# Kernel tuning notes

Measured on AMD Instinct MI355X. Metric: run time of the kernel, lower is better.

Reference implementation:

```python
import jax, jax.numpy as jnp
import numpy as np

B, L, D = 4, 1024, 1024
H, DK, DV = 16, 64, 64
HID = 4 * D
EPS = 1e-5


def layer_norm(x, w, b):
    m = x.mean(-1, keepdims=True)
    v = ((x - m) ** 2).mean(-1, keepdims=True)
    return (x - m) * jax.lax.rsqrt(v + EPS) * w + b


def sln(hl, w, ln_w, ln_b, gamma, beta):
    # Self-modulated LayerNorm: gamma * w * LN(hl) + beta * w
    return gamma * w * layer_norm(hl, ln_w, ln_b) + beta * w


def setup_inputs() -> dict:
    key = jax.random.key(0)
    ks = jax.random.split(key, 20)
    s = 0.02
    inp = {
        "q": jax.random.normal(ks[0], (B, L, D), jnp.float32),
        "k": jax.random.normal(ks[1], (B, L, D), jnp.float32),
        "v": jax.random.normal(ks[2], (B, L, D), jnp.float32),
        "z": jax.random.normal(ks[3], (B, L, D), jnp.float32),
        # projections stored [in, out] (torch Linear applies x @ W.T + b)
        "wq_w": jax.random.normal(ks[4], (D, H * DK), jnp.float32) * s,
        "wq_b": jnp.zeros((H * DK,), jnp.float32),
        "wk_w": jax.random.normal(ks[5], (D, H * DK), jnp.float32) * s,
        "wk_b": jnp.zeros((H * DK,), jnp.float32),
        "wv_w": jax.random.normal(ks[6], (D, H * DV), jnp.float32) * s,
        "wv_b": jnp.zeros((H * DV,), jnp.float32),
        "fc_w": jax.random.normal(ks[7], (H * DV, D), jnp.float32) * s,
        "fc_b": jnp.zeros((D,), jnp.float32),
        "mlp1_w": jax.random.normal(ks[8], (D, HID), jnp.float32) * s,
        "mlp1_b": jnp.zeros((HID,), jnp.float32),
        "mlp2_w": jax.random.normal(ks[9], (HID, D), jnp.float32) * s,
        "mlp2_b": jnp.zeros((D,), jnp.float32),
        "ln1_w": jnp.ones((D,), jnp.float32),
        "ln1_b": jnp.zeros((D,), jnp.float32),
        "g1": jax.random.normal(ks[10], (1, 1, 1), jnp.float32),
        "b1": jax.random.normal(ks[11], (1, 1, 1), jnp.float32),
        "ln2_w": jnp.ones((D,), jnp.float32),
        "ln2_b": jnp.zeros((D,), jnp.float32),
        "g2": jax.random.normal(ks[12], (1, 1, 1), jnp.float32),
        "b2": jax.random.normal(ks[13], (1, 1, 1), jnp.float32),
    }
    return inp


def reference(q, k, v, z,
              wq_w, wq_b, wk_w, wk_b, wv_w, wv_b, fc_w, fc_b,
              mlp1_w, mlp1_b, mlp2_w, mlp2_b,
              ln1_w, ln1_b, g1, b1, ln2_w, ln2_b, g2, b2):
    scale = 1.0 / np.sqrt(DK).astype(np.float32)
    q = sln(q, z, ln1_w, ln1_b, g1, b1)
    residual = q
    qh = (q @ wq_w + wq_b).reshape(B, L, H, DK)
    kh = (k @ wk_w + wk_b).reshape(B, L, H, DK)
    vh = (v @ wv_w + wv_b).reshape(B, L, H, DV)
    # scores per (head, batch) matching torch layout (n_head*sz_b, Lq, Lk)
    attn = jnp.einsum("bqhd,bkhd->hbqk", qh, kh) * scale
    attn = jax.nn.softmax(attn, axis=-1)
    out = jnp.einsum("hbqk,bkhd->bqhd", attn, vh).reshape(B, L, H * DV)
    out = out @ fc_w + fc_b
    out = out + residual
    h = sln(out, z, ln2_w, ln2_b, g2, b2)
    h = jax.nn.gelu(h @ mlp1_w + mlp1_b, approximate=False)
    out = (h @ mlp2_w + mlp2_b) + out
    return out, attn.reshape(H * B, L, L)
```

## Files before the change

### kernel.cpp

```cpp
#include <hip/hip_runtime.h>
#include <math.h>

namespace {

constexpr int kL  = 1024;
constexpr int kD  = 1024;
constexpr int kB  = 4;
constexpr int kH  = 16;
constexpr int kDK = 64;
constexpr int kHID = 4096;

typedef unsigned short ushort_t;
typedef short  s16x8 __attribute__((ext_vector_type(8)));
typedef float  f32x4 __attribute__((ext_vector_type(4)));
typedef unsigned short u16x4 __attribute__((ext_vector_type(4)));

__device__ __forceinline__ ushort_t f2bf(float f) {
    unsigned u = __float_as_uint(f);
    unsigned r = u + 0x7fffu + ((u >> 16) & 1u);
    return (ushort_t)(r >> 16);
}

__device__ __forceinline__ void gld16(const void* g, void* l) {
    __builtin_amdgcn_global_load_lds((__attribute__((address_space(1))) void*)(g),
                                     (__attribute__((address_space(3))) void*)(l),
                                     16, 0, 0);
}

__device__ __forceinline__ float wred_sum(float v) {
    #pragma unroll
    for (int o = 32; o > 0; o >>= 1) v += __shfl_xor(v, o, 64);
    return v;
}

__global__ __launch_bounds__(256) void prep(
    const float* __restrict__ wq_w, const float* __restrict__ wk_w,
    const float* __restrict__ wv_w, const float* __restrict__ fc_w,
    ushort_t* __restrict__ wT4,
    const float* __restrict__ mlp1_w, ushort_t* __restrict__ m1T,
    const float* __restrict__ mlp2_w, ushort_t* __restrict__ m2T,
    const float* __restrict__ kx, const float* __restrict__ vx, ushort_t* __restrict__ kv,
    const float* __restrict__ q, const float* __restrict__ z,
    const float* __restrict__ ln1w, const float* __restrict__ ln1b,
    const float* __restrict__ g1, const float* __restrict__ b1,
    float* __restrict__ qp, ushort_t* __restrict__ qb)
{
    __shared__ float t[32][33];
    __shared__ float r1[4], r2[4];
    const int b = blockIdx.x;
    const int tid = threadIdx.x;
    if (b < 12288) {
        const float* src; ushort_t* dst; int R, C, bx, by;
        if (b < 4096) {
            int zz = b >> 10, idx = b & 1023;
            src = zz == 0 ? wq_w : zz == 1 ? wk_w : zz == 2 ? wv_w : fc_w;
            dst = wT4 + (size_t)zz * 1048576;
            R = 1024; C = 1024; bx = idx & 31; by = idx >> 5;
        } else if (b < 8192) {
            int idx = b - 4096;
            src = mlp1_w; dst = m1T; R = 1024; C = 4096;
            bx = idx & 127; by = idx >> 7;
        } else {
            int idx = b - 8192;
            src = mlp2_w; dst = m2T; R = 4096; C = 1024;
            bx = idx & 31; by = idx >> 5;
        }
        int c0 = bx * 32, rr0 = by * 32;
        int tx = tid & 31, ty = tid >> 5;
        #pragma unroll
        for (int i = 0; i < 4; i++) {
            int r = ty + i * 8;
            t[r][tx] = src[(size_t)(rr0 + r) * C + c0 + tx];
        }
        __syncthreads();
        #pragma unroll
        for (int i = 0; i < 4; i++) {
            int c = ty + i * 8;
            dst[(size_t)(c0 + c) * R + rr0 + tx] = f2bf(t[tx][c]);
        }
        return;
    }
    if (b < 20480) {
        int bb = b - 12288;
        bool isv = bb >= 4096;
        const float* src = isv ? vx : kx;
        ushort_t* dst = kv + (isv ? (size_t)4194304 : 0);
        int i = (bb & 4095) * 256 + tid;
        f32x4 v = ((const f32x4*)src)[i];
        u16x4 o; o[0] = f2bf(v[0]); o[1] = f2bf(v[1]); o[2] = f2bf(v[2]); o[3] = f2bf(v[3]);
        ((u16x4*)dst)[i] = o;
        return;
    }
    {
        const int row = b - 20480;
        const size_t base = (size_t)row * kD;
        float4 xv = ((const float4*)(q + base))[tid];
        float s  = xv.x + xv.y + xv.z + xv.w;
        float sq = xv.x * xv.x + xv.y * xv.y + xv.z * xv.z + xv.w * xv.w;
        float ws = wred_sum(s), wq = wred_sum(sq);
        int lane = tid & 63, wid = tid >> 6;
        if (lane == 0) { r1[wid] = ws; r2[wid] = wq; }
        __syncthreads();
        float st = r1[0] + r1[1] + r1[2] + r1[3];
        float qt = r2[0] + r2[1] + r2[2] + r2[3];
        float mean = st * (1.0f / kD);
        float var  = qt * (1.0f / kD) - mean * mean;
        float rs = rsqrtf(var + 1e-5f);
        float gv = g1[0], bv = b1[0];
        float4 zv = ((const float4*)(z + base))[tid];
        float4 wv = ((const float4*)ln1w)[tid];
        float4 lb = ((const float4*)ln1b)[tid];
        float4 o;
        o.x = zv.x * (gv * ((xv.x - mean) * rs * wv.x + lb.x) + bv);
        o.y = zv.y * (gv * ((xv.y - mean) * rs * wv.y + lb.y) + bv);
        o.z = zv.z * (gv * ((xv.z - mean) * rs * wv.z + lb.z) + bv);
        o.w = zv.w * (gv * ((xv.w - mean) * rs * wv.w + lb.w) + bv);
        ((float4*)(qp + base))[tid] = o;
        u16x4 ob; ob[0] = f2bf(o.x); ob[1] = f2bf(o.y); ob[2] = f2bf(o.z); ob[3] = f2bf(o.w);
        ((u16x4*)(qb + base))[tid] = ob;
    }
}

__global__ __launch_bounds__(256) void sln_kernel(
    const float* __restrict__ x, const float* __restrict__ x2, float* __restrict__ xw,
    const float* __restrict__ z,
    const float* __restrict__ lnw, const float* __restrict__ lnb,
    const float* __restrict__ g, const float* __restrict__ bt,
    float* __restrict__ outf, ushort_t* __restrict__ outb)
{
    const int row = blockIdx.x;
    const int tid = threadIdx.x;
    const size_t base = (size_t)row * kD;
    float4 xv = ((const float4*)(x + base))[tid];
    if (x2) {
        float4 a = ((const float4*)(x2 + base))[tid];
        xv.x += a.x; xv.y += a.y; xv.z += a.z; xv.w += a.w;
    }
    if (xw) ((float4*)(xw + base))[tid] = xv;
    float s  = xv.x + xv.y + xv.z + xv.w;
    float sq = xv.x * xv.x + xv.y * xv.y + xv.z * xv.z + xv.w * xv.w;
    __shared__ float r1[4], r2[4];
    float ws = wred_sum(s), wq = wred_sum(sq);
    int lane = tid & 63, wid = tid >> 6;
    if (lane == 0) { r1[wid] = ws; r2[wid] = wq; }
    __syncthreads();
    float st = r1[0] + r1[1] + r1[2] + r1[3];
    float qt = r2[0] + r2[1] + r2[2] + r2[3];
    float mean = st * (1.0f / kD);
    float var  = qt * (1.0f / kD) - mean * mean;
    float rs = rsqrtf(var + 1e-5f);
    float gv = g[0], bv = bt[0];
    float4 zv = ((const float4*)(z + base))[tid];
    float4 wv = ((const float4*)lnw)[tid];
    float4 lb = ((const float4*)lnb)[tid];
    float4 o;
    o.x = zv.x * (gv * ((xv.x - mean) * rs * wv.x + lb.x) + bv);
    o.y = zv.y * (gv * ((xv.y - mean) * rs * wv.y + lb.y) + bv);
    o.z = zv.z * (gv * ((xv.z - mean) * rs * wv.z + lb.z) + bv);
    o.w = zv.w * (gv * ((xv.w - mean) * rs * wv.w + lb.w) + bv);
    if (outf) ((float4*)(outf + base))[tid] = o;
    u16x4 ob; ob[0] = f2bf(o.x); ob[1] = f2bf(o.y); ob[2] = f2bf(o.z); ob[3] = f2bf(o.w);
    ((u16x4*)(outb + base))[tid] = ob;
}

__global__ __launch_bounds__(256) void combine4(
    float* __restrict__ dst, const float* __restrict__ p1,
    const float* __restrict__ p2, const float* __restrict__ p3)
{
    int i = blockIdx.x * 256 + threadIdx.x;
    f32x4 d = ((const f32x4*)dst)[i];
    f32x4 a = ((const f32x4*)p1)[i];
    f32x4 b = ((const f32x4*)p2)[i];
    f32x4 c = ((const f32x4*)p3)[i];
    d[0] += a[0] + b[0] + c[0]; d[1] += a[1] + b[1] + c[1];
    d[2] += a[2] + b[2] + c[2]; d[3] += a[3] + b[3] + c[3];
    ((f32x4*)dst)[i] = d;
}

__global__ __launch_bounds__(256) void vtrans(
    const ushort_t* __restrict__ vh, ushort_t* __restrict__ vhT)
{
    __shared__ ushort_t t[32][33];
    int p = blockIdx.z, b = p & 3, h = p >> 2;
    int j0 = blockIdx.x * 32, d0 = blockIdx.y * 32;
    int tx = threadIdx.x & 31, ty = threadIdx.x >> 5;
    const ushort_t* src = vh + (size_t)b * (kL * kD) + h * kDK;
    #pragma unroll
    for (int i = 0; i < 4; i++) {
        int j = ty + i * 8;
        t[j][tx] = src[(size_t)(j0 + j) * kD + d0 + tx];
    }
    __syncthreads();
    ushort_t* dst = vhT + (size_t)p * (kDK * kL);
    #pragma unroll
    for (int i = 0; i < 4; i++) {
        int d = ty + i * 8;
        dst[(size_t)(d0 + d) * kL + j0 + tx] = t[tx][d];
    }
}

__global__ __launch_bounds__(256) void mgemm(
    const ushort_t* __restrict__ A, int lda,
    const ushort_t* __restrict__ Bt, int ldb,
    void* __restrict__ Cv, int ldc, int K,
    const float* __restrict__ bias, const float* __restrict__ res,
    float scale, int flags, int mode,
    const float* __restrict__ bias1, const float* __restrict__ bias2,
    void* __restrict__ Cv2)
{
    __shared__ __align__(16) ushort_t As[128 * 32];
    __shared__ __align__(16) ushort_t Bs[128 * 32];
    if (mode == 3) {
        int z = blockIdx.z;
        A  += (size_t)z * K;
        Bt += (size_t)z * K;
        if (z == 1) { Cv = Cv2; bias = nullptr; res = nullptr; flags = 0; }
    }
    float*    Cf = (float*)Cv;
    ushort_t* Cb = (ushort_t*)Cv;
    const int nx = gridDim.x, nwg = nx * gridDim.y;
    int f = blockIdx.y * nx + blockIdx.x;
    int rr = (f & 7) * (nwg >> 3) + (f >> 3);
    const int bx = rr % nx, by = rr / nx;
    const int tid = threadIdx.x;
    const int lane = tid & 63, w = tid >> 6;
    const int m0 = by * 128, n0 = bx * 128;
    const int r0 = tid >> 2;
    const int c0 = (tid & 3) ^ (r0 & 3);
    const ushort_t* Ag0 = A  + (size_t)(m0 + r0) * lda + c0 * 8;
    const ushort_t* Ag1 = Ag0 + (size_t)64 * lda;
    const ushort_t* Bg0 = Bt + (size_t)(n0 + r0) * ldb + c0 * 8;
    const ushort_t* Bg1 = Bg0 + (size_t)64 * ldb;
    char* AsW = (char*)As + w * 1024;
    char* BsW = (char*)Bs + w * 1024;
    const int wm = (w & 1) * 64, wn = (w >> 1) * 64;
    const int fn = lane & 15, q = lane >> 4;
    int aoff[4], boff[4];
    #pragma unroll
    for (int i = 0; i < 4; i++) {
        int ra = wm + i * 16 + fn;
        aoff[i] = (ra * 4 + (q ^ (ra & 3))) * 16;
        int rb = wn + i * 16 + fn;
        boff[i] = (rb * 4 + (q ^ (rb & 3))) * 16;
    }
    f32x4 acc[4][4] = {};
    for (int k0 = 0; k0 < K; k0 += 32) {
        gld16(Ag0 + k0, AsW);
        gld16(Ag1 + k0, AsW + 4096);
        gld16(Bg0 + k0, BsW);
        gld16(Bg1 + k0, BsW + 4096);
        __syncthreads();
        s16x8 af[4], bfr[4];
        #pragma unroll
        for (int i = 0; i < 4; i++) {
            af[i]  = *(const s16x8*)((const char*)As + aoff[i]);
            bfr[i] = *(const s16x8*)((const char*)Bs + boff[i]);
        }
        #pragma unroll
        for (int mi = 0; mi < 4; mi++)
            #pragma unroll
            for (int ni = 0; ni < 4; ni++)
                acc[mi][ni] = __builtin_amdgcn_mfma_f32_16x16x32_bf16(
                    af[mi], bfr[ni], acc[mi][ni], 0, 0, 0);
        __syncthreads();
    }
    #pragma unroll
    for (int mi = 0; mi < 4; mi++) {
        #pragma unroll
        for (int ni = 0; ni < 4; ni++) {
            #pragma unroll
            for (int r = 0; r < 4; r++) {
                int gm = m0 + wm + mi * 16 + q * 4 + r;
                int gn = n0 + wn + ni * 16 + fn;
                float v = acc[mi][ni][r] * scale;
                if (bias) v += bias[gn];
                if (flags & 1) v = 0.5f * v * (1.0f + erff(v * 0.70710678118654752f));
                if (res) v += res[(size_t)gm * ldc + gn];
                if (flags & 2) Cb[(size_t)gm * ldc + gn] = f2bf(v);
                else           Cf[(size_t)gm * ldc + gn] = v;
            }
        }
    }
}

__global__ __launch_bounds__(512, 2) void g3(
    const ushort_t* __restrict__ A, int lda,
    const ushort_t* __restrict__ Bt, int ldb,
    void* __restrict__ Cv, int ldc, int K,
    const float* __restrict__ bias, const float* __restrict__ res,
    float scale, int flags, int mode,
    const float* __restrict__ bias1, const float* __restrict__ bias2,
    float* __restrict__ Cv2, float* __restrict__ Cv3)
{
    __shared__ __align__(16) ushort_t As[3 * 8192];
    __shared__ __align__(16) ushort_t Bs[3 * 8192];
    if (mode == 2) {
        int zz = blockIdx.z;
        A  += (size_t)zz * (4096u * 1024u);
        Bt += (size_t)zz * (1024u * 1024u);
        Cv = (void*)((ushort_t*)Cv + (size_t)zz * (4096u * 1024u));
        if (zz == 1) bias = bias1;
        else if (zz == 2) bias = bias2;
    } else if (mode == 4) {
        int zz = blockIdx.z;
        A  += (size_t)zz * K;
        Bt += (size_t)zz * K;
        if (zz > 0) {
            Cv = (void*)(zz == 3 ? Cv3 : (Cv2 + (size_t)(zz - 1) * (4096u * 1024u)));
            bias = nullptr; res = nullptr; flags = 0;
        }
    }
    float*    Cf = (float*)Cv;
    ushort_t* Cb = (ushort_t*)Cv;
    const int nx = gridDim.x, nwg = nx * gridDim.y;
    int f = blockIdx.y * nx + blockIdx.x;
    int rr = (f & 7) * (nwg >> 3) + (f >> 3);
    const int bx = rr % nx, by = rr / nx;
    const int tid = threadIdx.x;
    const int lane = tid & 63, w = tid >> 6;
    const int wr = w >> 2, wc = w & 3;
    const int fn = lane & 15, q = lane >> 4;
    const int m0 = by * 256, n0 = bx * 256;
    const int r0 = tid >> 2;
    const int c0 = (tid & 3) ^ (r0 & 3);
    const ushort_t* Ag = A  + (size_t)(m0 + r0) * lda + c0 * 8;
    const ushort_t* Bg = Bt + (size_t)(n0 + r0) * ldb + c0 * 8;
    char* AsB = (char*)As;
    char* BsB = (char*)Bs;
    const int sdst = w * 1024;
    int aoff[8], boff[4];
    #pragma unroll
    for (int i = 0; i < 8; i++) {
        int ra = wr * 128 + i * 16 + fn;
        aoff[i] = ra * 64 + ((q ^ (ra & 3)) << 4);
    }
    #pragma unroll
    for (int i = 0; i < 4; i++) {
        int rb = wc * 64 + i * 16 + fn;
        boff[i] = rb * 64 + ((q ^ (rb & 3)) << 4);
    }
    const int NT = K >> 5;
    f32x4 acc[8][4] = {};

    #define G3_STAGE(T, s_, h_)                                                   \
        do {                                                                      \
            gld16(Ag + (size_t)((h_) * 128) * lda + (size_t)(T) * 32,             \
                  AsB + (s_) * 16384 + (h_) * 8192 + sdst);                       \
            gld16(Bg + (size_t)((h_) * 128) * ldb + (size_t)(T) * 32,             \
                  BsB + (s_) * 16384 + (h_) * 8192 + sdst);                       \
        } while (0)

    G3_STAGE(0, 0, 0); G3_STAGE(0, 0, 1);
    G3_STAGE(1, 1, 0); G3_STAGE(1, 1, 1);
    asm volatile("s_waitcnt vmcnt(4)" ::: "memory");
    __builtin_amdgcn_s_barrier();
    __builtin_amdgcn_sched_barrier(0);

    int sT = 0, s2 = 2;
    for (int T = 0; T < NT; ++T) {
        if (T + 2 < NT) { G3_STAGE(T + 2, s2, 0); G3_STAGE(T + 2, s2, 1); }
        const char* Asl = (const char*)As + sT * 16384;
        const char* Bsl = (const char*)Bs + sT * 16384;
        s16x8 af[8], bf[4];
        #pragma unroll
        for (int i = 0; i < 8; i++) af[i] = *(const s16x8*)(Asl + aoff[i]);
        #pragma unroll
        for (int i = 0; i < 4; i++) bf[i] = *(const s16x8*)(Bsl + boff[i]);
        asm volatile("s_waitcnt lgkmcnt(0)" ::: "memory");
        __builtin_amdgcn_sched_barrier(0);
        __builtin_amdgcn_s_setprio(1);
        #pragma unroll
        for (int mi = 0; mi < 8; mi++)
            #pragma unroll
            for (int ni = 0; ni < 4; ni++)
                acc[mi][ni] = __builtin_amdgcn_mfma_f32_16x16x32_bf16(
                    af[mi], bf[ni], acc[mi][ni], 0, 0, 0);
        __builtin_amdgcn_s_setprio(0);
        __builtin_amdgcn_sched_barrier(0);
        if (T + 1 < NT) {
            if (T + 2 < NT) asm volatile("s_waitcnt vmcnt(4)" ::: "memory");
            else            asm volatile("s_waitcnt vmcnt(0)" ::: "memory");
            __builtin_amdgcn_s_barrier();
            __builtin_amdgcn_sched_barrier(0);
        }
        sT = (sT == 2) ? 0 : sT + 1;
        s2 = (s2 == 2) ? 0 : s2 + 1;
    }
    #undef G3_STAGE

    #pragma unroll
    for (int mi = 0; mi < 8; mi++) {
        #pragma unroll
        for (int ni = 0; ni < 4; ni++) {
            #pragma unroll
            for (int r = 0; r < 4; r++) {
                int gm = m0 + wr * 128 + mi * 16 + q * 4 + r;
                int gn = n0 + wc * 64 + ni * 16 + fn;
                float v = acc[mi][ni][r] * scale;
                if (bias) v += bias[gn];
                if (flags & 1) v = 0.5f * v * (1.0f + erff(v * 0.70710678118654752f));
                if (res) v += res[(size_t)gm * ldc + gn];
                if (flags & 2) Cb[(size_t)gm * ldc + gn] = f2bf(v);
                else           Cf[(size_t)gm * ldc + gn] = v;
            }
        }
    }
}

__global__ __launch_bounds__(512) void fused_attn(
    const ushort_t* __restrict__ qh, const ushort_t* __restrict__ kh,
    const ushort_t* __restrict__ vhT, float* __restrict__ attn,
    ushort_t* __restrict__ ctx)
{
    __shared__ __align__(16) char PlBuf[8 * 4096];
    __shared__ float redm[8][32];
    __shared__ float reds[8][32];
    const int orig = blockIdx.y * 32 + blockIdx.x;
    const int nf = (orig & 7) * 256 + (orig >> 3);
    const int p = nf >> 5, b = p & 3, h = p >> 2;
    const int m0 = (nf & 31) * 32;
    const int tid = threadIdx.x;
    const int lane = tid & 63, w = tid >> 6;
    const int fn = lane & 15, q = lane >> 4;
    const ushort_t* Qb = qh + (size_t)b * (kL * kD) + h * 64;
    const ushort_t* Kb = kh + (size_t)b * (kL * kD) + h * 64;
    float* Pp = attn + (size_t)p * kL * kL;

    f32x4 acc[2][8] = {};
    #pragma unroll
    for (int kk = 0; kk < 2; kk++) {
        s16x8 aq[2], bq[8];
        #pragma unroll
        for (int mi = 0; mi < 2; mi++)
            aq[mi] = *(const s16x8*)(Qb + (size_t)(m0 + mi * 16 + fn) * kD + kk * 32 + q * 8);
        #pragma unroll
        for (int ni = 0; ni < 8; ni++)
            bq[ni] = *(const s16x8*)(Kb + (size_t)(w * 128 + ni * 16 + fn) * kD + kk * 32 + q * 8);
        #pragma unroll
        for (int mi = 0; mi < 2; mi++)
            #pragma unroll
            for (int ni = 0; ni < 8; ni++)
                acc[mi][ni] = __builtin_amdgcn_mfma_f32_16x16x32_bf16(
                    aq[mi], bq[ni], acc[mi][ni], 0, 0, 0);
    }

    float mloc[2][4];
    #pragma unroll
    for (int mi = 0; mi < 2; mi++) {
        #pragma unroll
        for (int r = 0; r < 4; r++) {
            float m = -3.0e38f;
            #pragma unroll
            for (int ni = 0; ni < 8; ni++) {
                acc[mi][ni][r] *= 0.125f;
                m = fmaxf(m, acc[mi][ni][r]);
            }
            mloc[mi][r] = m;
        }
    }
    #pragma unroll
    for (int o = 1; o < 16; o <<= 1) {
        #pragma unroll
        for (int mi = 0; mi < 2; mi++)
            #pragma unroll
            for (int r = 0; r < 4; r++)
                mloc[mi][r] = fmaxf(mloc[mi][r], __shfl_xor(mloc[mi][r], o, 64));
    }
    if (fn == 0) {
        #pragma unroll
        for (int mi = 0; mi < 2; mi++)
            #pragma unroll
            for (int r = 0; r < 4; r++)
                redm[w][mi * 16 + q * 4 + r] = mloc[mi][r];
    }
    __syncthreads();
    #pragma unroll
    for (int mi = 0; mi < 2; mi++) {
        #pragma unroll
        for (int r = 0; r < 4; r++) {
            int row = mi * 16 + q * 4 + r;
            float m = redm[0][row];
            #pragma unroll
            for (int w2 = 1; w2 < 8; w2++) m = fmaxf(m, redm[w2][row]);
            float s = 0.f;
            #pragma unroll
            for (int ni = 0; ni < 8; ni++) {
                float e = __expf(acc[mi][ni][r] - m);
                acc[mi][ni][r] = e;
                s += e;
            }
            mloc[mi][r] = s;
        }
    }
    #pragma unroll
    for (int o = 1; o < 16; o <<= 1) {
        #pragma unroll
        for (int mi = 0; mi < 2; mi++)
            #pragma unroll
            for (int r = 0; r < 4; r++)
                mloc[mi][r] += __shfl_xor(mloc[mi][r], o, 64);
    }
    if (fn == 0) {
        #pragma unroll
        for (int mi = 0; mi < 2; mi++)
            #pragma unroll
            for (int r = 0; r < 4; r++)
                reds[w][mi * 16 + q * 4 + r] = mloc[mi][r];
    }
    __syncthreads();
    float inv[2][4];
    #pragma unroll
    for (int mi = 0; mi < 2; mi++) {
        #pragma unroll
        for (int r = 0; r < 4; r++) {
            int row = mi * 16 + q * 4 + r;
            float s = reds[0][row];
            #pragma unroll
            for (int w2 = 1; w2 < 8; w2++) s += reds[w2][row];
            inv[mi][r] = 1.0f / s;
        }
    }
    #pragma unroll
    for (int mi = 0; mi < 2; mi++)
        #pragma unroll
        for (int ni = 0; ni < 8; ni++)
            #pragma unroll
            for (int r = 0; r < 4; r++)
                __builtin_nontemporal_store(
                    acc[mi][ni][r] * inv[mi][r],
                    &Pp[(size_t)(m0 + mi * 16 + q * 4 + r) * kL + w * 128 + ni * 16 + fn]);

    const ushort_t* Vb = vhT + (size_t)p * (kDK * kL);
    char* Plw = PlBuf + w * 4096;
    f32x4 acc2[2][4] = {};
    #pragma unroll
    for (int half = 0; half < 2; half++) {
        #pragma unroll
        for (int mi = 0; mi < 2; mi++)
            #pragma unroll
            for (int ni = 0; ni < 4; ni++)
                #pragma unroll
                for (int r = 0; r < 4; r++) {
                    int row = mi * 16 + q * 4 + r;
                    int cl  = ni * 16 + fn;
                    *(ushort_t*)(Plw + ((row * 128 + cl * 2) ^ ((row & 7) << 4)))
                        = f2bf(acc[mi][half * 4 + ni][r]);
                }
        #pragma unroll
        for (int kh2 = 0; kh2 < 2; kh2++) {
            int kk = half * 2 + kh2;
            s16x8 pa[2];
            #pragma unroll
            for (int mi = 0; mi < 2; mi++) {
                int row = mi * 16 + fn;
                pa[mi] = *(const s16x8*)(Plw +
                    ((row * 128 + (kh2 * 32 + q * 8) * 2) ^ ((row & 7) << 4)));
            }
            #pragma unroll
            for (int nj = 0; nj < 4; nj++) {
                s16x8 bv = *(const s16x8*)(Vb + (size_t)(nj * 16 + fn) * kL +
                                           w * 128 + kk * 32 + q * 8);
                #pragma unroll
                for (int mi = 0; mi < 2; mi++)
                    acc2[mi][nj] = __builtin_amdgcn_mfma_f32_16x16x32_bf16(
                        pa[mi], bv, acc2[mi][nj], 0, 0, 0);
            }
        }
    }
    #pragma unroll
    for (int mi = 0; mi < 2; mi++)
        #pragma unroll
        for (int nj = 0; nj < 4; nj++)
            #pragma unroll
            for (int r = 0; r < 4; r++)
                acc2[mi][nj][r] *= inv[mi][r];

    __syncthreads();
    float (*cred)[2048] = (float (*)[2048])PlBuf;
    if (w < 4) {
        #pragma unroll
        for (int mi = 0; mi < 2; mi++)
            #pragma unroll
            for (int nj = 0; nj < 4; nj++)
                #pragma unroll
                for (int r = 0; r < 4; r++)
                    cred[w][(mi * 16 + q * 4 + r) * 64 + nj * 16 + fn] = acc2[mi][nj][r];
    }
    __syncthreads();
    if (w >= 4) {
        #pragma unroll
        for (int mi = 0; mi < 2; mi++)
            #pragma unroll
            for (int nj = 0; nj < 4; nj++)
                #pragma unroll
                for (int r = 0; r < 4; r++)
                    cred[w - 4][(mi * 16 + q * 4 + r) * 64 + nj * 16 + fn] += acc2[mi][nj][r];
    }
    __syncthreads();
    {
        int idx0 = tid * 4;
        int row = idx0 >> 6, d0 = idx0 & 63;
        f32x4 s0 = *(const f32x4*)&cred[0][idx0];
        #pragma unroll
        for (int wb = 1; wb < 4; wb++) {
            f32x4 t = *(const f32x4*)&cred[wb][idx0];
            s0[0] += t[0]; s0[1] += t[1]; s0[2] += t[2]; s0[3] += t[3];
        }
        u16x4 o;
        o[0] = f2bf(s0[0]); o[1] = f2bf(s0[1]); o[2] = f2bf(s0[2]); o[3] = f2bf(s0[3]);
        *(u16x4*)(ctx + (size_t)b * (kL * kD) + (size_t)(m0 + row) * kD + h * 64 + d0) = o;
    }
}

}

extern "C" void kernel_launch(void* const* d_in, const int* in_sizes, int n_in,
                              void* d_out, int out_size, void* d_ws, size_t ws_size,
                              hipStream_t stream)
{
    (void)in_sizes; (void)n_in; (void)out_size; (void)ws_size;
    const float* q      = (const float*)d_in[0];
    const float* k      = (const float*)d_in[1];
    const float* v      = (const float*)d_in[2];
    const float* z      = (const float*)d_in[3];
    const float* wq_w   = (const float*)d_in[4];
    const float* wq_b   = (const float*)d_in[5];
    const float* wk_w   = (const float*)d_in[6];
    const float* wk_b   = (const float*)d_in[7];
    const float* wv_w   = (const float*)d_in[8];
    const float* wv_b   = (const float*)d_in[9];
    const float* fc_w   = (const float*)d_in[10];
    const float* fc_b   = (const float*)d_in[11];
    const float* mlp1_w = (const float*)d_in[12];
    const float* mlp1_b = (const float*)d_in[13];
    const float* mlp2_w = (const float*)d_in[14];
    const float* mlp2_b = (const float*)d_in[15];
    const float* ln1_w  = (const float*)d_in[16];
    const float* ln1_b  = (const float*)d_in[17];
    const float* g1     = (const float*)d_in[18];
    const float* b1     = (const float*)d_in[19];
    const float* ln2_w  = (const float*)d_in[20];
    const float* ln2_b  = (const float*)d_in[21];
    const float* g2     = (const float*)d_in[22];
    const float* b2     = (const float*)d_in[23];

    float* out0 = (float*)d_out;
    float* attn = (float*)d_out + (size_t)kB * kL * kD;

    char* arena = (char*)d_ws;
    const size_t MB = 1u << 20;
    float*    qp   = (float*)(arena);
    ushort_t* qb   = (ushort_t*)(arena + 16 * MB);
    ushort_t* kb   = (ushort_t*)(arena + 24 * MB);
    ushort_t* vb   = (ushort_t*)(arena + 32 * MB);
    ushort_t* qh   = (ushort_t*)(arena + 40 * MB);
    ushort_t* kh   = (ushort_t*)(arena + 48 * MB);
    ushort_t* vh   = (ushort_t*)(arena + 56 * MB);
    ushort_t* vhT  = (ushort_t*)(arena + 32 * MB);
    ushort_t* ctx  = (ushort_t*)(arena + 56 * MB);
    float*    fcP  = (float*)(arena + 16 * MB);
    ushort_t* h2   = (ushort_t*)(arena + 32 * MB);
    float*    out1 = (float*)(arena + 64 * MB);
    ushort_t* hid  = (ushort_t*)(arena);
    float*    p1   = (float*)(arena + 32 * MB);
    float*    p3   = (float*)(arena + 80 * MB);
    ushort_t* wT4  = (ushort_t*)(arena + 80 * MB);
    ushort_t* fcT  = (ushort_t*)(arena + 86 * MB);
    ushort_t* m1T  = (ushort_t*)(arena + 88 * MB);
    ushort_t* m2T  = (ushort_t*)(arena + 96 * MB);

    dim3 blk(256);
    prep<<<dim3(24576), blk, 0, stream>>>(wq_w, wk_w, wv_w, fc_w, wT4,
                                          mlp1_w, m1T, mlp2_w, m2T,
                                          k, v, kb,
                                          q, z, ln1_w, ln1_b, g1, b1, qp, qb);
    g3<<<dim3(4, 16, 3), dim3(512), 0, stream>>>(qb, kD, wT4, kD, qh, kD, kD,
                                                 wq_b, nullptr, 1.0f, 2, 2,
                                                 wk_b, wv_b, nullptr, nullptr);
    vtrans<<<dim3(32, 2, 64), blk, 0, stream>>>(vh, vhT);
    fused_attn<<<dim3(kL / 32, 64), dim3(512), 0, stream>>>(qh, kh, vhT, attn, ctx);
    mgemm<<<dim3(8, 32, 2), blk, 0, stream>>>(ctx, kD, fcT, kD, out1, kD, kD / 2,
                                              fc_b, qp, 1.0f, 0, 3, nullptr, nullptr, fcP);
    sln_kernel<<<dim3(kB * kL), blk, 0, stream>>>(out1, fcP, out1, z,
                                                  ln2_w, ln2_b, g2, b2, nullptr, h2);
    g3<<<dim3(16, 16, 1), dim3(512), 0, stream>>>(h2, kD, m1T, kD, hid, kHID, kD,
                                                  mlp1_b, nullptr, 1.0f, 3, 0,
                                                  nullptr, nullptr, nullptr, nullptr);
    g3<<<dim3(4, 16, 4), dim3(512), 0, stream>>>(hid, kHID, m2T, kHID, out0, kD, kHID / 4,
                                                 mlp2_b, out1, 1.0f, 0, 4,
                                                 nullptr, nullptr, p1, p3);
    combine4<<<dim3(4096), blk, 0, stream>>>(out0, p1, p1 + (size_t)4096 * 1024, p3);
}
```

Before: 822.3 us.

## Replace g3 GEMM with 8-phase ping-pong K=64 pipelined g8 kernel

Replaces the 3-stage K=32 GEMM with a new kernel that uses K=64 tiles, double-buffered 128KB LDS, and splits each tile's MFMA work into eight quadrant phases. Global-to-LDS loads and LDS reads are interleaved between those phases, with a barrier around each, so memory traffic overlaps compute. The LDS swizzle is widened to 8 chunks to match the 128-byte rows. Occupancy drops to one block per CU because of the LDS size, and the extra barriers add synchronisation cost.

```diff
diff --git a/kernel.cpp b/kernel.cpp
--- a/kernel.cpp
+++ b/kernel.cpp
@@ -205,16 +205,15 @@
     void* __restrict__ Cv, int ldc, int K,
     const float* __restrict__ bias, const float* __restrict__ res,
     float scale, int flags, int mode,
-    const float* __restrict__ bias1, const float* __restrict__ bias2,
-    void* __restrict__ Cv2)
+    const float* __restrict__ bias1, void* __restrict__ Cv2)
 {
     __shared__ __align__(16) ushort_t As[128 * 32];
     __shared__ __align__(16) ushort_t Bs[128 * 32];
     if (mode == 3) {
-        int z = blockIdx.z;
-        A  += (size_t)z * K;
-        Bt += (size_t)z * K;
-        if (z == 1) { Cv = Cv2; bias = nullptr; res = nullptr; flags = 0; }
+        int zz = blockIdx.z;
+        A  += (size_t)zz * K;
+        Bt += (size_t)zz * K;
+        if (zz == 1) { Cv = Cv2; bias = nullptr; res = nullptr; flags = 0; }
     }
     float*    Cf = (float*)Cv;
     ushort_t* Cb = (ushort_t*)Cv;
@@ -283,22 +282,49 @@
     }
 }
 
-__global__ __launch_bounds__(512, 2) void g3(
+#define G8_PRE()  do { __builtin_amdgcn_sched_barrier(0); __builtin_amdgcn_s_barrier(); \
+    asm volatile("s_waitcnt lgkmcnt(0)" ::: "memory"); \
+    __builtin_amdgcn_sched_barrier(0); __builtin_amdgcn_s_setprio(1); } while (0)
+#define G8_POST() do { __builtin_amdgcn_s_setprio(0); __builtin_amdgcn_sched_barrier(0); \
+    __builtin_amdgcn_s_barrier(); } while (0)
+#define STG_A(T, h, base) do { \
+    const ushort_t* _s = Aga + (size_t)(T) * 64 + (size_t)((h) * 64) * lda; \
+    gld16(_s, (base) + (h) * 16384 + sdst); \
+    gld16(_s + (size_t)128 * lda, (base) + (h) * 16384 + 8192 + sdst); } while (0)
+#define STG_B(T, h, base) do { \
+    const ushort_t* _s = Bga + (size_t)(T) * 64 + (size_t)((h) * 32) * ldb; \
+    gld16(_s, (base) + (h) * 16384 + sdst); \
+    gld16(_s + (size_t)128 * ldb, (base) + (h) * 16384 + 8192 + sdst); } while (0)
+#define RD_A(base, half) do { _Pragma("unroll") \
+    for (int i = 0; i < 4; i++) { \
+        af[i][0] = *(const s16x8*)((base) + (half) * 16384 + aoff[i] + xoff0); \
+        af[i][1] = *(const s16x8*)((base) + (half) * 16384 + aoff[i] + xoff1); } } while (0)
+#define RD_B(dst, base, half) do { _Pragma("unroll") \
+    for (int j = 0; j < 2; j++) { \
+        dst[j][0] = *(const s16x8*)((base) + (half) * 16384 + boff[j] + xoff0); \
+        dst[j][1] = *(const s16x8*)((base) + (half) * 16384 + boff[j] + xoff1); } } while (0)
+#define QUAD(MB, NB, BF) do { _Pragma("unroll") \
+    for (int ks = 0; ks < 2; ks++) { _Pragma("unroll") \
+        for (int mi = 0; mi < 4; mi++) { _Pragma("unroll") \
+            for (int ni = 0; ni < 2; ni++) \
+                acc[(MB) + mi][(NB) + ni] = __builtin_amdgcn_mfma_f32_16x16x32_bf16( \
+                    af[mi][ks], BF[ni][ks], acc[(MB) + mi][(NB) + ni], 0, 0, 0); } } } while (0)
+
+__global__ __launch_bounds__(512, 1) void g8(
     const ushort_t* __restrict__ A, int lda,
     const ushort_t* __restrict__ Bt, int ldb,
     void* __restrict__ Cv, int ldc, int K,
     const float* __restrict__ bias, const float* __restrict__ res,
-    float scale, int flags, int mode,
+    int flags, int mode,
     const float* __restrict__ bias1, const float* __restrict__ bias2,
-    float* __restrict__ Cv2, float* __restrict__ Cv3)
+    float* __restrict__ Cp1, float* __restrict__ Cp2, float* __restrict__ Cp3)
 {
-    __shared__ __align__(16) ushort_t As[3 * 8192];
-    __shared__ __align__(16) ushort_t Bs[3 * 8192];
+    __shared__ __align__(16) char lds[131072];
     if (mode == 2) {
         int zz = blockIdx.z;
-        A  += (size_t)zz * (4096u * 1024u);
-        Bt += (size_t)zz * (1024u * 1024u);
-        Cv = (void*)((ushort_t*)Cv + (size_t)zz * (4096u * 1024u));
+        A  += (size_t)zz * 4194304u;
+        Bt += (size_t)zz * 1048576u;
+        Cv = (void*)((ushort_t*)Cv + (size_t)zz * 4194304u);
         if (zz == 1) bias = bias1;
         else if (zz == 2) bias = bias2;
     } else if (mode == 4) {
@@ -306,7 +332,7 @@
         A  += (size_t)zz * K;
         Bt += (size_t)zz * K;
         if (zz > 0) {
-            Cv = (void*)(zz == 3 ? Cv3 : (Cv2 + (size_t)(zz - 1) * (4096u * 1024u)));
+            Cv = (void*)(zz == 1 ? Cp1 : zz == 2 ? Cp2 : Cp3);
             bias = nullptr; res = nullptr; flags = 0;
         }
     }
@@ -321,72 +347,65 @@
     const int wr = w >> 2, wc = w & 3;
     const int fn = lane & 15, q = lane >> 4;
     const int m0 = by * 256, n0 = bx * 256;
-    const int r0 = tid >> 2;
-    const int c0 = (tid & 3) ^ (r0 & 3);
-    const ushort_t* Ag = A  + (size_t)(m0 + r0) * lda + c0 * 8;
-    const ushort_t* Bg = Bt + (size_t)(n0 + r0) * ldb + c0 * 8;
-    char* AsB = (char*)As;
-    char* BsB = (char*)Bs;
+    const int ar = w * 8 + (lane >> 3);
+    const int cb = ((lane & 7) ^ ((lane >> 3) & 7)) * 8;
+    const int br0 = ((ar >> 5) << 6) + (ar & 31);
+    const ushort_t* Aga = A  + (size_t)(m0 + ar)  * lda + cb;
+    const ushort_t* Bga = Bt + (size_t)(n0 + br0) * ldb + cb;
     const int sdst = w * 1024;
-    int aoff[8], boff[4];
-    #pragma unroll
-    for (int i = 0; i < 8; i++) {
-        int ra = wr * 128 + i * 16 + fn;
-        aoff[i] = ra * 64 + ((q ^ (ra & 3)) << 4);
-    }
-    #pragma unroll
-    for (int i = 0; i < 4; i++) {
-        int rb = wc * 64 + i * 16 + fn;
-        boff[i] = rb * 64 + ((q ^ (rb & 3)) << 4);
-    }
-    const int NT = K >> 5;
+    char* const Ab0 = lds;
+    char* const Bb0 = lds + 32768;
+    char* const Ab1 = lds + 65536;
+    char* const Bb1 = lds + 98304;
+    const int xoff0 = ((q)     ^ (fn & 7)) << 4;
+    const int xoff1 = ((4 + q) ^ (fn & 7)) << 4;
+    int aoff[4], boff[2];
+    #pragma unroll
+    for (int i = 0; i < 4; i++) aoff[i] = ((i << 4) + fn + wr * 64) * 128;
+    #pragma unroll
+    for (int j = 0; j < 2; j++) boff[j] = ((j << 4) + fn + wc * 32) * 128;
+
+    const int NT = K >> 6;
     f32x4 acc[8][4] = {};
-
-    #define G3_STAGE(T, s_, h_)                                                   \
-        do {                                                                      \
-            gld16(Ag + (size_t)((h_) * 128) * lda + (size_t)(T) * 32,             \
-                  AsB + (s_) * 16384 + (h_) * 8192 + sdst);                       \
-            gld16(Bg + (size_t)((h_) * 128) * ldb + (size_t)(T) * 32,             \
-                  BsB + (s_) * 16384 + (h_) * 8192 + sdst);                       \
-        } while (0)
-
-    G3_STAGE(0, 0, 0); G3_STAGE(0, 0, 1);
-    G3_STAGE(1, 1, 0); G3_STAGE(1, 1, 1);
-    asm volatile("s_waitcnt vmcnt(4)" ::: "memory");
+    s16x8 af[4][2], bf01[2][2], bf23[2][2];
+
+    STG_A(0, 0, Ab0); STG_A(0, 1, Ab0); STG_B(0, 0, Bb0); STG_B(0, 1, Bb0);
+    STG_A(1, 0, Ab1); STG_B(1, 0, Bb1); STG_B(1, 1, Bb1);
+    asm volatile("s_waitcnt vmcnt(6)" ::: "memory");
     __builtin_amdgcn_s_barrier();
     __builtin_amdgcn_sched_barrier(0);
 
-    int sT = 0, s2 = 2;
-    for (int T = 0; T < NT; ++T) {
-        if (T + 2 < NT) { G3_STAGE(T + 2, s2, 0); G3_STAGE(T + 2, s2, 1); }
-        const char* Asl = (const char*)As + sT * 16384;
-        const char* Bsl = (const char*)Bs + sT * 16384;
-        s16x8 af[8], bf[4];
-        #pragma unroll
-        for (int i = 0; i < 8; i++) af[i] = *(const s16x8*)(Asl + aoff[i]);
-        #pragma unroll
-        for (int i = 0; i < 4; i++) bf[i] = *(const s16x8*)(Bsl + boff[i]);
-        asm volatile("s_waitcnt lgkmcnt(0)" ::: "memory");
-        __builtin_amdgcn_sched_barrier(0);
-        __builtin_amdgcn_s_setprio(1);
-        #pragma unroll
-        for (int mi = 0; mi < 8; mi++)
-            #pragma unroll
-            for (int ni = 0; ni < 4; ni++)
-                acc[mi][ni] = __builtin_amdgcn_mfma_f32_16x16x32_bf16(
-                    af[mi], bf[ni], acc[mi][ni], 0, 0, 0);
-        __builtin_amdgcn_s_setprio(0);
-        __builtin_amdgcn_sched_barrier(0);
-        if (T + 1 < NT) {
-            if (T + 2 < NT) asm volatile("s_waitcnt vmcnt(4)" ::: "memory");
-            else            asm volatile("s_waitcnt vmcnt(0)" ::: "memory");
-            __builtin_amdgcn_s_barrier();
-            __builtin_amdgcn_sched_barrier(0);
-        }
-        sT = (sT == 2) ? 0 : sT + 1;
-        s2 = (s2 == 2) ? 0 : s2 + 1;
-    }
-    #undef G3_STAGE
+    for (int it = 0; it < (NT >> 1); ++it) {
+        const int t0 = it << 1, t1 = t0 | 1;
+        const bool s2 = (t0 + 2) < NT;
+        const bool s3 = (t0 + 3) < NT;
+        STG_A(t1, 1, Ab1);
+        RD_A(Ab0, 0); RD_B(bf01, Bb0, 0);
+        G8_PRE(); QUAD(0, 0, bf01); G8_POST();
+        if (s2) STG_A(t0 + 2, 0, Ab0);
+        RD_B(bf23, Bb0, 1);
+        G8_PRE(); QUAD(0, 2, bf23); G8_POST();
+        if (s2) STG_B(t0 + 2, 0, Bb0);
+        RD_A(Ab0, 1);
+        G8_PRE(); QUAD(4, 0, bf01); G8_POST();
+        if (s2) STG_B(t0 + 2, 1, Bb0);
+        if (s2) asm volatile("s_waitcnt vmcnt(6)" ::: "memory");
+        else    asm volatile("s_waitcnt vmcnt(0)" ::: "memory");
+        G8_PRE(); QUAD(4, 2, bf23); G8_POST();
+        if (s2) STG_A(t0 + 2, 1, Ab0);
+        RD_A(Ab1, 0); RD_B(bf01, Bb1, 0);
+        G8_PRE(); QUAD(0, 0, bf01); G8_POST();
+        if (s3) STG_A(t0 + 3, 0, Ab1);
+        RD_B(bf23, Bb1, 1);
+        G8_PRE(); QUAD(0, 2, bf23); G8_POST();
+        if (s3) STG_B(t0 + 3, 0, Bb1);
+        RD_A(Ab1, 1);
+        G8_PRE(); QUAD(4, 0, bf01); G8_POST();
+        if (s3) STG_B(t0 + 3, 1, Bb1);
+        if (s3) asm volatile("s_waitcnt vmcnt(6)" ::: "memory");
+        else    asm volatile("s_waitcnt vmcnt(0)" ::: "memory");
+        G8_PRE(); QUAD(4, 2, bf23); G8_POST();
+    }
 
     #pragma unroll
     for (int mi = 0; mi < 8; mi++) {
@@ -396,7 +415,7 @@
             for (int r = 0; r < 4; r++) {
                 int gm = m0 + wr * 128 + mi * 16 + q * 4 + r;
                 int gn = n0 + wc * 64 + ni * 16 + fn;
-                float v = acc[mi][ni][r] * scale;
+                float v = acc[mi][ni][r];
                 if (bias) v += bias[gn];
                 if (flags & 1) v = 0.5f * v * (1.0f + erff(v * 0.70710678118654752f));
                 if (res) v += res[(size_t)gm * ldc + gn];
@@ -663,6 +682,7 @@
     float*    out1 = (float*)(arena + 64 * MB);
     ushort_t* hid  = (ushort_t*)(arena);
     float*    p1   = (float*)(arena + 32 * MB);
+    float*    p2   = (float*)(arena + 48 * MB);
     float*    p3   = (float*)(arena + 80 * MB);
     ushort_t* wT4  = (ushort_t*)(arena + 80 * MB);
     ushort_t* fcT  = (ushort_t*)(arena + 86 * MB);
@@ -674,20 +694,20 @@
                                           mlp1_w, m1T, mlp2_w, m2T,
                                           k, v, kb,
                                           q, z, ln1_w, ln1_b, g1, b1, qp, qb);
-    g3<<<dim3(4, 16, 3), dim3(512), 0, stream>>>(qb, kD, wT4, kD, qh, kD, kD,
-                                                 wq_b, nullptr, 1.0f, 2, 2,
-                                                 wk_b, wv_b, nullptr, nullptr);
+    g8<<<dim3(4, 16, 3), dim3(512), 0, stream>>>(qb, kD, wT4, kD, qh, kD, kD,
+                                                 wq_b, nullptr, 2, 2, wk_b, wv_b,
+                                                 nullptr, nullptr, nullptr);
     vtrans<<<dim3(32, 2, 64), blk, 0, stream>>>(vh, vhT);
     fused_attn<<<dim3(kL / 32, 64), dim3(512), 0, stream>>>(qh, kh, vhT, attn, ctx);
     mgemm<<<dim3(8, 32, 2), blk, 0, stream>>>(ctx, kD, fcT, kD, out1, kD, kD / 2,
-                                              fc_b, qp, 1.0f, 0, 3, nullptr, nullptr, fcP);
+                                              fc_b, qp, 1.0f, 0, 3, nullptr, fcP);
     sln_kernel<<<dim3(kB * kL), blk, 0, stream>>>(out1, fcP, out1, z,
                                                   ln2_w, ln2_b, g2, b2, nullptr, h2);
-    g3<<<dim3(16, 16, 1), dim3(512), 0, stream>>>(h2, kD, m1T, kD, hid, kHID, kD,
-                                                  mlp1_b, nullptr, 1.0f, 3, 0,
-                                                  nullptr, nullptr, nullptr, nullptr);
-    g3<<<dim3(4, 16, 4), dim3(512), 0, stream>>>(hid, kHID, m2T, kHID, out0, kD, kHID / 4,
-                                                 mlp2_b, out1, 1.0f, 0, 4,
-                                                 nullptr, nullptr, p1, p3);
-    combine4<<<dim3(4096), blk, 0, stream>>>(out0, p1, p1 + (size_t)4096 * 1024, p3);
-}
+    g8<<<dim3(16, 16, 1), dim3(512), 0, stream>>>(h2, kD, m1T, kD, hid, kHID, kD,
+                                                  mlp1_b, nullptr, 3, 0, nullptr, nullptr,
+                                                  nullptr, nullptr, nullptr);
+    g8<<<dim3(4, 16, 4), dim3(512), 0, stream>>>(hid, kHID, m2T, kHID, out0, kD, kHID / 4,
+                                                 mlp2_b, out1, 0, 4, nullptr, nullptr,
+                                                 p1, p2, p3);
+    combine4<<<dim3(4096), blk, 0, stream>>>(out0, p1, p2, p3);
+}
```

After: 902.8 us. 1.1x slower.
